# Optimization experiments

Hardware: AMD Instinct MI355X
Metric: run time of the kernel (lower is better)

The kernel has to match this reference:

```python
import jax, jax.numpy as jnp
import numpy as np

# Dims: node hidden = (VO vectors, SO scalars); messages = (VEC_IN vectors, S_M scalars)
VO, SO, VEC_IN, S_M = 16, 100, 17, 132
B, N, K = 4, 2048, 30


def _split(x, nv):
    # flat [..., 3*nv + ns] -> vectors [..., 3, nv], scalars [..., ns]
    v = x[..., :3 * nv].reshape(x.shape[:-1] + (3, nv))
    return v, x[..., 3 * nv:]


def _merge(v, s):
    return jnp.concatenate([v.reshape(v.shape[:-2] + (3 * v.shape[-1],)), s], -1)


def _norm_no_nan(x, axis=-1, keepdims=False, eps=1e-8, sqrt=True):
    out = jnp.maximum(jnp.sum(x * x, axis=axis, keepdims=keepdims), eps)
    return jnp.sqrt(out) if sqrt else out


def _vs_concat(x1, x2, nv1, nv2):
    v1, s1 = _split(x1, nv1)
    v2, s2 = _split(x2, nv2)
    return _merge(jnp.concatenate([v1, v2], -1), jnp.concatenate([s1, s2], -1))


def _gvp(x, nv_in, wh, ws, bs, wv, act=True):
    # Geometric Vector Perceptron: nls=relu on scalars, nlv=sigmoid gate on vector norms.
    v, s = _split(x, nv_in)
    vh = jnp.einsum('...ci,ih->...ch', v, wh)        # c = 3 spatial dims
    vn = _norm_no_nan(vh, axis=-2)                    # [..., h]
    s_out = jnp.concatenate([s, vn], -1) @ ws + bs
    if act:
        s_out = jax.nn.relu(s_out)
    v_out = jnp.einsum('...ch,ho->...co', vh, wv)
    if act:
        v_out = v_out * jax.nn.sigmoid(_norm_no_nan(v_out, axis=-2, keepdims=True))
    return _merge(v_out, s_out)


def _gvp_layernorm(x, nv, gamma, beta, eps=1e-3):
    # scalars: standard LayerNorm (keras default eps=1e-3); vectors: divide by RMS of channel norms
    v, s = _split(x, nv)
    vn2 = _norm_no_nan(v, axis=-2, keepdims=True, sqrt=False)      # [..., 1, nv]
    v = v / jnp.sqrt(jnp.mean(vn2, axis=-1, keepdims=True))
    mu = jnp.mean(s, -1, keepdims=True)
    var = jnp.mean((s - mu) ** 2, -1, keepdims=True)
    s = (s - mu) * jax.lax.rsqrt(var + eps) * gamma + beta
    return _merge(v, s)


def _dense(key, fan_in, fan_out):
    return jax.random.normal(key, (fan_in, fan_out), jnp.float32) / np.sqrt(fan_in)


def setup_inputs() -> dict:
    key = jax.random.key(0)
    ks = jax.random.split(key, 20)
    d = {
        'h_V': jax.random.normal(ks[0], (B, N, 3 * VO + SO), jnp.float32),
        'h_M': jax.random.normal(ks[1], (B, N, K, 3 * VEC_IN + S_M), jnp.float32),
        'mask_V': jnp.ones((B, N), jnp.int32),
        'mask_attend': jnp.ones((B, N, K), jnp.int32),
    }
    # W_EV: GVP(33->16, 232->100), GVP(16->16, 100->100), GVP(16->16, 100->100, no act)
    d['wev1_wh'] = _dense(ks[2], 33, 33)
    d['wev1_ws'] = _dense(ks[3], 232 + 33, 100)
    d['wev1_bs'] = jnp.zeros((100,), jnp.float32)
    d['wev1_wv'] = _dense(ks[4], 33, 16)
    d['wev2_wh'] = _dense(ks[5], 16, 16)
    d['wev2_ws'] = _dense(ks[6], 116, 100)
    d['wev2_bs'] = jnp.zeros((100,), jnp.float32)
    d['wev2_wv'] = _dense(ks[7], 16, 16)
    d['wev3_wh'] = _dense(ks[8], 16, 16)
    d['wev3_ws'] = _dense(ks[9], 116, 100)
    d['wev3_bs'] = jnp.zeros((100,), jnp.float32)
    d['wev3_wv'] = _dense(ks[10], 16, 16)
    # W_dh: GVP(16->32, 100->400), GVP(32->16, 400->100, no act)
    d['wdh1_wh'] = _dense(ks[11], 16, 32)
    d['wdh1_ws'] = _dense(ks[12], 100 + 32, 400)
    d['wdh1_bs'] = jnp.zeros((400,), jnp.float32)
    d['wdh1_wv'] = _dense(ks[13], 32, 32)
    d['wdh2_wh'] = _dense(ks[14], 32, 32)
    d['wdh2_ws'] = _dense(ks[15], 400 + 32, 100)
    d['wdh2_bs'] = jnp.zeros((100,), jnp.float32)
    d['wdh2_wv'] = _dense(ks[16], 32, 16)
    d['ln1_g'] = jnp.ones((100,), jnp.float32)
    d['ln1_b'] = jnp.zeros((100,), jnp.float32)
    d['ln2_g'] = jnp.ones((100,), jnp.float32)
    d['ln2_b'] = jnp.zeros((100,), jnp.float32)
    return d


def reference(h_V, h_M, mask_V, mask_attend,
              wev1_wh, wev1_ws, wev1_bs, wev1_wv,
              wev2_wh, wev2_ws, wev2_bs, wev2_wv,
              wev3_wh, wev3_ws, wev3_bs, wev3_wv,
              wdh1_wh, wdh1_ws, wdh1_bs, wdh1_wv,
              wdh2_wh, wdh2_ws, wdh2_bs, wdh2_wv,
              ln1_g, ln1_b, ln2_g, ln2_b):
    # tile node features along neighbor axis, concat with messages
    h_V_exp = jnp.broadcast_to(h_V[..., None, :], h_M.shape[:-1] + (h_V.shape[-1],))
    h_EV = _vs_concat(h_V_exp, h_M, VO, VEC_IN)                   # [B,N,K, 3*33 + 232]
    m = _gvp(h_EV, VO + VEC_IN, wev1_wh, wev1_ws, wev1_bs, wev1_wv)
    m = _gvp(m, VO, wev2_wh, wev2_ws, wev2_bs, wev2_wv)
    m = _gvp(m, VO, wev3_wh, wev3_ws, wev3_bs, wev3_wv, act=False)
    m = mask_attend[..., None].astype(jnp.float32) * m
    dh = jnp.mean(m, axis=-2)                                     # reduce over neighbors
    hv = _gvp_layernorm(h_V + dh, VO, ln1_g, ln1_b)               # dropout inactive (train=False)
    dh = _gvp(hv, VO, wdh1_wh, wdh1_ws, wdh1_bs, wdh1_wv)
    dh = _gvp(dh, 2 * VO, wdh2_wh, wdh2_ws, wdh2_bs, wdh2_wv, act=False)
    hv = _gvp_layernorm(hv + dh, VO, ln2_g, ln2_b)
    return mask_V[..., None].astype(jnp.float32) * hv
```

## Files before the change

### kernel.cpp

```cpp
#include <hip/hip_runtime.h>
#include <math.h>

#define NT 256

typedef __attribute__((ext_vector_type(8))) short short8;
typedef __attribute__((ext_vector_type(4))) float float4v;

struct P28 {
    const float *h_V, *h_M;
    const int *mask_V, *mask_attend;
    const float *w1h,*w1s,*b1,*w1v;
    const float *w2h,*w2s,*b2,*w2v;
    const float *w3h,*w3s,*b3,*w3v;
    const float *d1h,*d1s,*db1,*d1v;
    const float *d2h,*d2s,*db2,*d2v;
    const float *g1,*be1,*g2,*be2;
    float *out, *dh;
    short *wt1, *wt2, *wt3;
};

__device__ inline short f2bf(float f) {
    union { float f; unsigned u; } v; v.f = f;
    unsigned r = (v.u + 0x7FFFu + ((v.u >> 16) & 1u)) >> 16;
    return (short)r;
}

__device__ void gemm(const float* A0, int split, const float* A1, int KA,
                     const float* uni, int uniK,
                     const float* Bg, int ldB, int N,
                     const float* bias, bool relu,
                     float* outL, int MP, float* Bbuf, int bbf, int tid)
{
    const bool vec = ((N & 3) == 0) && ((ldB & 3) == 0);
    const int Npad = vec ? N : ((N + 3) & ~3);
    const int EQ = MP >> 2;
    const int npairs = EQ * (Npad >> 2);
    const int Ktot = uniK + KA;
    int KC = bbf / Npad;
    if (KC > Ktot) KC = Ktot;

    const bool active = tid < npairs;
    const int e0 = (active ? (tid % EQ) : 0) * 4;
    const int j0 = (active ? (tid / EQ) : 0) * 4;

    float c00=0.f,c01=0.f,c02=0.f,c03=0.f;
    float c10=0.f,c11=0.f,c12=0.f,c13=0.f;
    float c20=0.f,c21=0.f,c22=0.f,c23=0.f;
    float c30=0.f,c31=0.f,c32=0.f,c33=0.f;
    float su0=0.f,su1=0.f,su2=0.f,su3=0.f;

    float4 r0, r1, r2, r3;
    r0.x=r0.y=r0.z=r0.w=0.f; r1=r0; r2=r0; r3=r0;

    if (vec) {
        int kc0 = (KC < Ktot) ? KC : Ktot;
        int nf4 = (kc0 * N) >> 2;
        int f4 = tid;
        if (f4 < nf4) { int f = f4*4; int k = f / N; r0 = *(const float4*)(Bg + (size_t)k*ldB + (f - k*N)); }
        f4 = tid + NT;
        if (f4 < nf4) { int f = f4*4; int k = f / N; r1 = *(const float4*)(Bg + (size_t)k*ldB + (f - k*N)); }
        f4 = tid + 2*NT;
        if (f4 < nf4) { int f = f4*4; int k = f / N; r2 = *(const float4*)(Bg + (size_t)k*ldB + (f - k*N)); }
        f4 = tid + 3*NT;
        if (f4 < nf4) { int f = f4*4; int k = f / N; r3 = *(const float4*)(Bg + (size_t)k*ldB + (f - k*N)); }
    }

    for (int k0 = 0; k0 < Ktot; k0 += KC) {
        int kc = Ktot - k0; if (kc > KC) kc = KC;
        __syncthreads();
        if (vec) {
            int nf4 = (kc * N) >> 2;
            float4* Bb4 = (float4*)Bbuf;
            if (tid        < nf4) Bb4[tid]        = r0;
            if (tid +   NT < nf4) Bb4[tid +   NT] = r1;
            if (tid + 2*NT < nf4) Bb4[tid + 2*NT] = r2;
            if (tid + 3*NT < nf4) Bb4[tid + 3*NT] = r3;
            int k0n = k0 + KC;
            if (k0n < Ktot) {
                int kcn = Ktot - k0n; if (kcn > KC) kcn = KC;
                int nf4n = (kcn * N) >> 2;
                const float* Bn = Bg + (size_t)k0n * ldB;
                int f4 = tid;
                if (f4 < nf4n) { int f = f4*4; int k = f / N; r0 = *(const float4*)(Bn + (size_t)k*ldB + (f - k*N)); }
                f4 = tid + NT;
                if (f4 < nf4n) { int f = f4*4; int k = f / N; r1 = *(const float4*)(Bn + (size_t)k*ldB + (f - k*N)); }
                f4 = tid + 2*NT;
                if (f4 < nf4n) { int f = f4*4; int k = f / N; r2 = *(const float4*)(Bn + (size_t)k*ldB + (f - k*N)); }
                f4 = tid + 3*NT;
                if (f4 < nf4n) { int f = f4*4; int k = f / N; r3 = *(const float4*)(Bn + (size_t)k*ldB + (f - k*N)); }
            }
        } else {
            for (int idx = tid; idx < kc * Npad; idx += NT) {
                int k = idx / Npad, j = idx - k * Npad;
                Bbuf[idx] = (j < N) ? Bg[(size_t)(k0 + k) * ldB + j] : 0.f;
            }
        }
        __syncthreads();
        if (active) {
            for (int k = 0; k < kc; ++k) {
                int kg = k0 + k;
                float4 b4 = *(const float4*)(Bbuf + k * Npad + j0);
                if (kg < uniK) {
                    float u = uni[kg];
                    su0 = fmaf(u, b4.x, su0); su1 = fmaf(u, b4.y, su1);
                    su2 = fmaf(u, b4.z, su2); su3 = fmaf(u, b4.w, su3);
                } else {
                    int ka = kg - uniK;
                    const float* arow = (ka < split) ? (A0 + (size_t)ka * MP + e0)
                                                     : (A1 + (size_t)(ka - split) * MP + e0);
                    float4 a4 = *(const float4*)arow;
                    c00 = fmaf(a4.x, b4.x, c00); c01 = fmaf(a4.y, b4.x, c01);
                    c02 = fmaf(a4.z, b4.x, c02); c03 = fmaf(a4.w, b4.x, c03);
                    c10 = fmaf(a4.x, b4.y, c10); c11 = fmaf(a4.y, b4.y, c11);
                    c12 = fmaf(a4.z, b4.y, c12); c13 = fmaf(a4.w, b4.y, c13);
                    c20 = fmaf(a4.x, b4.z, c20); c21 = fmaf(a4.y, b4.z, c21);
                    c22 = fmaf(a4.z, b4.z, c22); c23 = fmaf(a4.w, b4.z, c23);
                    c30 = fmaf(a4.x, b4.w, c30); c31 = fmaf(a4.y, b4.w, c31);
                    c32 = fmaf(a4.z, b4.w, c32); c33 = fmaf(a4.w, b4.w, c33);
                }
            }
        }
    }
    __syncthreads();
    if (active) {
        float4 o;
        if (j0 + 0 < N) {
            float s = su0 + (bias ? bias[j0 + 0] : 0.f);
            o.x = c00 + s; o.y = c01 + s; o.z = c02 + s; o.w = c03 + s;
            if (relu) { o.x = fmaxf(o.x,0.f); o.y = fmaxf(o.y,0.f); o.z = fmaxf(o.z,0.f); o.w = fmaxf(o.w,0.f); }
            *(float4*)(outL + (size_t)(j0 + 0) * MP + e0) = o;
        }
        if (j0 + 1 < N) {
            float s = su1 + (bias ? bias[j0 + 1] : 0.f);
            o.x = c10 + s; o.y = c11 + s; o.z = c12 + s; o.w = c13 + s;
            if (relu) { o.x = fmaxf(o.x,0.f); o.y = fmaxf(o.y,0.f); o.z = fmaxf(o.z,0.f); o.w = fmaxf(o.w,0.f); }
            *(float4*)(outL + (size_t)(j0 + 1) * MP + e0) = o;
        }
        if (j0 + 2 < N) {
            float s = su2 + (bias ? bias[j0 + 2] : 0.f);
            o.x = c20 + s; o.y = c21 + s; o.z = c22 + s; o.w = c23 + s;
            if (relu) { o.x = fmaxf(o.x,0.f); o.y = fmaxf(o.y,0.f); o.z = fmaxf(o.z,0.f); o.w = fmaxf(o.w,0.f); }
            *(float4*)(outL + (size_t)(j0 + 2) * MP + e0) = o;
        }
        if (j0 + 3 < N) {
            float s = su3 + (bias ? bias[j0 + 3] : 0.f);
            o.x = c30 + s; o.y = c31 + s; o.z = c32 + s; o.w = c33 + s;
            if (relu) { o.x = fmaxf(o.x,0.f); o.y = fmaxf(o.y,0.f); o.z = fmaxf(o.z,0.f); o.w = fmaxf(o.w,0.f); }
            *(float4*)(outL + (size_t)(j0 + 3) * MP + e0) = o;
        }
    }
}

__device__ void vn_dev(const float* vh, int nch, int MP, int cs,
                       float* out, int ostr, int tid)
{
    for (int idx = tid; idx < nch * cs; idx += NT) {
        int h = idx / cs, e = idx - h * cs;
        float a = vh[h * MP + e], b = vh[h * MP + cs + e], c = vh[h * MP + 2 * cs + e];
        out[h * ostr + e] = sqrtf(fmaxf(a * a + b * b + c * c, 1e-8f));
    }
}

__device__ void gate_dev(float* vb, int nch, int MP, int cs, int tid)
{
    for (int idx = tid; idx < nch * cs; idx += NT) {
        int o = idx / cs, e = idx - o * cs;
        float* b = vb + o * MP + e;
        float a = b[0], b1 = b[cs], c = b[2 * cs];
        float n = sqrtf(fmaxf(a * a + b1 * b1 + c * c, 1e-8f));
        float g = 1.f / (1.f + expf(-n));
        b[0] = a * g; b[cs] = b1 * g; b[2 * cs] = c * g;
    }
}

__device__ void mfma_gemm(const short* Alds, int Astr, const short* Bg, int Kpad,
                          int ktiles, const float* bias,
                          short* outA, int outAstr, float* outS, int tid)
{
    const int w = tid >> 6, lane = tid & 63;
    const int q = lane >> 4, l16 = lane & 15;
    for (int t = w; t < 14; t += 4) {
        int mt = t & 1, nt = t >> 1;
        const short* ap = Alds + (mt * 16 + l16) * Astr + q * 8;
        const short* bp = Bg + (size_t)(nt * 16 + l16) * Kpad + q * 8;
        float4v acc = {0.f, 0.f, 0.f, 0.f};
        for (int kt = 0; kt < ktiles; ++kt) {
            short8 a = *(const short8*)(ap + kt * 32);
            short8 b = *(const short8*)(bp + kt * 32);
            acc = __builtin_amdgcn_mfma_f32_16x16x32_bf16(a, b, acc, 0, 0, 0);
        }
        int j = nt * 16 + l16;
        if (j < 100) {
            float bj = bias ? bias[j] : 0.f;
            int ebase = mt * 16 + q * 4;
            for (int r = 0; r < 4; ++r) {
                float v = acc[r] + bj;
                if (outA) { v = fmaxf(v, 0.f); outA[(ebase + r) * outAstr + j] = f2bf(v); }
                else      { outS[j * 33 + (ebase + r)] = v; }
            }
        }
    }
}

__global__ __launch_bounds__(NT) void prep_w(P28 p)
{
    int id = blockIdx.x * NT + threadIdx.x;
    int stride = gridDim.x * NT;
    for (int i = id; i < 112 * 288; i += stride) {
        int n = i / 288, k = i - n * 288;
        float v = 0.f;
        if (n < 100) {
            int row = -1;
            if (k < 132) row = 100 + k;
            else if (k < 165) row = 232 + (k - 132);
            else if (k < 265) row = k - 165;
            if (row >= 0) v = p.w1s[(size_t)row * 100 + n];
        }
        p.wt1[i] = f2bf(v);
    }
    for (int i = id; i < 112 * 128; i += stride) {
        int n = i / 128, k = i - n * 128;
        p.wt2[i] = f2bf((n < 100 && k < 116) ? p.w2s[(size_t)k * 100 + n] : 0.f);
    }
    for (int i = id; i < 112 * 128; i += stride) {
        int n = i / 128, k = i - n * 128;
        p.wt3[i] = f2bf((n < 100 && k < 116) ? p.w3s[(size_t)k * 100 + n] : 0.f);
    }
}

__global__ __launch_bounds__(NT) void edge_kernel(P28 p)
{
    __shared__ __align__(16) float Bbuf[1200];
    __shared__ __align__(16) short A1s[32 * 296];
    __shared__ __align__(16) float bufY[3300];
    __shared__ __align__(16) float vhb[33 * 96];
    __shared__ float maskf[32];

    short* A3s = A1s;
    short* A2s = (short*)bufY;
    float* vbuf = bufY;
    float* S3   = bufY;

    const int node = blockIdx.x, tid = threadIdx.x;
    const float* hV = p.h_V + (size_t)node * 148;

    for (int i = tid; i < 32; i += NT)
        maskf[i] = (i < 30) ? (float)p.mask_attend[(size_t)node * 30 + i] : 0.f;
    for (int idx = tid; idx < 32 * 132; idx += NT) {
        int e = idx / 132, k = idx - e * 132;
        float v = (e < 30) ? p.h_M[((size_t)node * 30 + e) * 183 + 51 + k] : 0.f;
        A1s[e * 296 + k] = f2bf(v);
    }
    for (int idx = tid; idx < 32 * 100; idx += NT) {
        int i = idx >> 5, e = idx & 31;
        A1s[e * 296 + 165 + i] = f2bf(hV[48 + i]);
    }
    for (int idx = tid; idx < 32 * 23; idx += NT) {
        int kk = idx / 32, e = idx - kk * 32;
        A1s[e * 296 + 265 + kk] = 0;
    }
    for (int idx = tid; idx < 33 * 96; idx += NT) {
        int i = idx / 96, r = idx - i * 96, c = r >> 5, e = r & 31;
        float v = 0.f;
        if (i < 16) v = hV[c * 16 + i];
        else if (e < 30) v = p.h_M[((size_t)node * 30 + e) * 183 + c * 17 + (i - 16)];
        vbuf[idx] = v;
    }
    __syncthreads();

    gemm(vbuf, 33, nullptr, 33, nullptr, 0, p.w1h, 33, 33, nullptr, false, vhb, 96, Bbuf, 1200, tid);
    __syncthreads();
    for (int idx = tid; idx < 33 * 32; idx += NT) {
        int h = idx >> 5, e = idx & 31;
        float a = vhb[h * 96 + e], b = vhb[h * 96 + 32 + e], c = vhb[h * 96 + 64 + e];
        A1s[e * 296 + 132 + h] = f2bf(sqrtf(fmaxf(a * a + b * b + c * c, 1e-8f)));
    }
    for (int idx = tid; idx < 32 * 12; idx += NT) {
        int kk = idx >> 5, e = idx & 31;
        A2s[e * 136 + 116 + kk] = 0;
    }
    __syncthreads();
    gemm(vhb, 33, nullptr, 33, nullptr, 0, p.w1v, 16, 16, nullptr, false, vhb, 96, Bbuf, 1200, tid);
    __syncthreads();
    gate_dev(vhb, 16, 96, 32, tid);
    __syncthreads();
    mfma_gemm(A1s, 296, p.wt1, 288, 9, p.b1, A2s, 136, nullptr, tid);
    __syncthreads();

    gemm(vhb, 16, nullptr, 16, nullptr, 0, p.w2h, 16, 16, nullptr, false, vhb + 16 * 96, 96, Bbuf, 1200, tid);
    __syncthreads();
    for (int idx = tid; idx < 16 * 32; idx += NT) {
        int h = idx >> 5, e = idx & 31;
        float a = vhb[(16 + h) * 96 + e], b = vhb[(16 + h) * 96 + 32 + e], c = vhb[(16 + h) * 96 + 64 + e];
        A2s[e * 136 + 100 + h] = f2bf(sqrtf(fmaxf(a * a + b * b + c * c, 1e-8f)));
    }
    for (int idx = tid; idx < 32 * 12; idx += NT) {
        int kk = idx >> 5, e = idx & 31;
        A3s[e * 136 + 116 + kk] = 0;
    }
    __syncthreads();
    gemm(vhb + 16 * 96, 16, nullptr, 16, nullptr, 0, p.w2v, 16, 16, nullptr, false, vhb, 96, Bbuf, 1200, tid);
    __syncthreads();
    gate_dev(vhb, 16, 96, 32, tid);
    __syncthreads();
    mfma_gemm(A2s, 136, p.wt2, 128, 4, p.b2, A3s, 136, nullptr, tid);
    __syncthreads();

    gemm(vhb, 16, nullptr, 16, nullptr, 0, p.w3h, 16, 16, nullptr, false, vhb + 16 * 96, 96, Bbuf, 1200, tid);
    __syncthreads();
    for (int idx = tid; idx < 16 * 32; idx += NT) {
        int h = idx >> 5, e = idx & 31;
        float a = vhb[(16 + h) * 96 + e], b = vhb[(16 + h) * 96 + 32 + e], c = vhb[(16 + h) * 96 + 64 + e];
        A3s[e * 136 + 100 + h] = f2bf(sqrtf(fmaxf(a * a + b * b + c * c, 1e-8f)));
    }
    __syncthreads();
    gemm(vhb + 16 * 96, 16, nullptr, 16, nullptr, 0, p.w3v, 16, 16, nullptr, false, vhb, 96, Bbuf, 1200, tid);
    __syncthreads();
    mfma_gemm(A3s, 136, p.wt3, 128, 4, p.b3, nullptr, 0, S3, tid);
    __syncthreads();

    float* dhn = p.dh + (size_t)node * 148;
    for (int f = tid; f < 148; f += NT) {
        float s = 0.f;
        int e = f % 30;
        if (f < 48) {
            int c = f >> 4, o = f & 15;
            const float* src = vhb + o * 96 + c * 32;
            for (int t = 0; t < 30; ++t) { s += maskf[e] * src[e]; if (++e == 30) e = 0; }
        } else {
            const float* src = S3 + (size_t)(f - 48) * 33;
            for (int t = 0; t < 30; ++t) { s += maskf[e] * src[e]; if (++e == 30) e = 0; }
        }
        dhn[f] = s * (1.f / 30.f);
    }
}

__global__ __launch_bounds__(NT) void node_kernel(P28 p)
{
    __shared__ __align__(16) float Bbuf[3200];
    __shared__ __align__(16) float S1n[132 * 16];
    __shared__ __align__(16) float A2n[400 * 16];
    __shared__ __align__(16) float s2n[100 * 16];
    __shared__ __align__(16) float hvv[16 * 48];
    __shared__ __align__(16) float vhA[32 * 48];
    __shared__ __align__(16) float vhB[32 * 48];
    __shared__ float mu[16], isd[16], vrm[16], mkv[16];

    const int nb = blockIdx.x * 16;
    const int tid = threadIdx.x;

    for (int idx = tid; idx < 1600; idx += NT) {
        int n = idx & 15, j = idx >> 4;
        size_t g = (size_t)(nb + n) * 148 + 48 + j;
        S1n[idx] = p.h_V[g] + p.dh[g];
    }
    for (int idx = tid; idx < 768; idx += NT) {
        int i = idx / 48, r = idx - i * 48, c = r >> 4, n = r & 15;
        size_t g = (size_t)(nb + n) * 148 + c * 16 + i;
        hvv[idx] = p.h_V[g] + p.dh[g];
    }
    for (int i = tid; i < 16; i += NT) mkv[i] = (float)p.mask_V[nb + i];
    __syncthreads();

    if (tid < 16) {
        int n = tid;
        float sm = 0.f;
        for (int j = 0; j < 100; ++j) sm += S1n[j * 16 + n];
        float m = sm * 0.01f, var = 0.f;
        for (int j = 0; j < 100; ++j) { float d = S1n[j * 16 + n] - m; var += d * d; }
        mu[n] = m; isd[n] = rsqrtf(var * 0.01f + 1e-3f);
        float vm = 0.f;
        for (int i = 0; i < 16; ++i) {
            float a = hvv[i * 48 + n], b = hvv[i * 48 + 16 + n], c = hvv[i * 48 + 32 + n];
            vm += fmaxf(a * a + b * b + c * c, 1e-8f);
        }
        vrm[n] = rsqrtf(vm * (1.f / 16.f));
    }
    __syncthreads();
    for (int idx = tid; idx < 1600; idx += NT) {
        int n = idx & 15, j = idx >> 4;
        S1n[idx] = (S1n[idx] - mu[n]) * isd[n] * p.g1[j] + p.be1[j];
    }
    for (int idx = tid; idx < 768; idx += NT) hvv[idx] *= vrm[idx & 15];
    __syncthreads();

    gemm(hvv, 16, nullptr, 16, nullptr, 0, p.d1h, 32, 32, nullptr, false, vhA, 48, Bbuf, 3200, tid);
    __syncthreads();
    vn_dev(vhA, 32, 48, 16, S1n + 100 * 16, 16, tid);
    __syncthreads();
    gemm(S1n, 132, nullptr, 132, nullptr, 0, p.d1s,       400, 200, p.db1,       true, A2n,            16, Bbuf, 3200, tid);
    gemm(S1n, 132, nullptr, 132, nullptr, 0, p.d1s + 200, 400, 200, p.db1 + 200, true, A2n + 200 * 16, 16, Bbuf, 3200, tid);
    gemm(vhA, 32, nullptr, 32, nullptr, 0, p.d1v, 32, 32, nullptr, false, vhB, 48, Bbuf, 3200, tid);
    __syncthreads();
    gate_dev(vhB, 32, 48, 16, tid);
    __syncthreads();

    gemm(vhB, 32, nullptr, 32, nullptr, 0, p.d2h, 32, 32, nullptr, false, vhA, 48, Bbuf, 3200, tid);
    __syncthreads();
    vn_dev(vhA, 32, 48, 16, S1n + 100 * 16, 16, tid);
    __syncthreads();
    gemm(A2n, 400, S1n + 100 * 16, 432, nullptr, 0, p.d2s, 100, 100, p.db2, false, s2n, 16, Bbuf, 3200, tid);
    gemm(vhA, 32, nullptr, 32, nullptr, 0, p.d2v, 16, 16, nullptr, false, vhB, 48, Bbuf, 3200, tid);
    __syncthreads();

    for (int idx = tid; idx < 1600; idx += NT) s2n[idx] += S1n[idx];
    for (int idx = tid; idx < 768; idx += NT) vhB[idx] += hvv[idx];
    __syncthreads();

    if (tid < 16) {
        int n = tid;
        float sm = 0.f;
        for (int j = 0; j < 100; ++j) sm += s2n[j * 16 + n];
        float m = sm * 0.01f, var = 0.f;
        for (int j = 0; j < 100; ++j) { float d = s2n[j * 16 + n] - m; var += d * d; }
        mu[n] = m; isd[n] = rsqrtf(var * 0.01f + 1e-3f);
        float vm = 0.f;
        for (int i = 0; i < 16; ++i) {
            float a = vhB[i * 48 + n], b = vhB[i * 48 + 16 + n], c = vhB[i * 48 + 32 + n];
            vm += fmaxf(a * a + b * b + c * c, 1e-8f);
        }
        vrm[n] = rsqrtf(vm * (1.f / 16.f));
    }
    __syncthreads();
    for (int idx = tid; idx < 1600; idx += NT) {
        int n = idx & 15, j = idx >> 4;
        s2n[idx] = (s2n[idx] - mu[n]) * isd[n] * p.g2[j] + p.be2[j];
    }
    for (int idx = tid; idx < 768; idx += NT) vhB[idx] *= vrm[idx & 15];
    __syncthreads();

    for (int idx = tid; idx < 16 * 148; idx += NT) {
        int n = idx / 148, f = idx - n * 148;
        float v;
        if (f < 48) { int c = f >> 4, o = f & 15; v = vhB[o * 48 + c * 16 + n]; }
        else        { v = s2n[(f - 48) * 16 + n]; }
        p.out[(size_t)(nb + n) * 148 + f] = mkv[n] * v;
    }
}

extern "C" void kernel_launch(void* const* d_in, const int* in_sizes, int n_in,
                              void* d_out, int out_size, void* d_ws, size_t ws_size,
                              hipStream_t stream)
{
    P28 p;
    p.h_V = (const float*)d_in[0];
    p.h_M = (const float*)d_in[1];
    p.mask_V = (const int*)d_in[2];
    p.mask_attend = (const int*)d_in[3];
    const float** w = (const float**)&p.w1h;
    for (int i = 0; i < 24; ++i) w[i] = (const float*)d_in[4 + i];
    p.out = (float*)d_out;
    p.dh  = (float*)d_out;
    p.wt1 = (short*)d_ws;
    p.wt2 = p.wt1 + 112 * 288;
    p.wt3 = p.wt2 + 112 * 128;

    prep_w<<<dim3(64), dim3(NT), 0, stream>>>(p);
    edge_kernel<<<dim3(8192), dim3(NT), 0, stream>>>(p);
    node_kernel<<<dim3(512),  dim3(NT), 0, stream>>>(p);
}
```

Before: 778.2 us.

## Fold per-node scalar term into bias and read small weights directly from global

The node scalar features are identical across all 30 neighbors, so their contribution to the first GVP scalar layer is computed once per node as a bias vector (ubias). This shrinks the MFMA K dimension from 288 to 192. The staged shared-memory GEMM is replaced by gemm_d, which reads weight rows straight from global memory (with w1h padded to 36 columns in prep_w), and two barriers around gate_dev are removed. The cost is a per-node 100x100 fp32 dot-product loop run by only 100 threads, and more scattered global reads of the small weight matrices.

```diff
diff --git a/kernel.cpp b/kernel.cpp
--- a/kernel.cpp
+++ b/kernel.cpp
@@ -17,6 +17,7 @@
     const float *g1,*be1,*g2,*be2;
     float *out, *dh;
     short *wt1, *wt2, *wt3;
+    float *wp1h;
 };
 
 __device__ inline short f2bf(float f) {
@@ -151,6 +152,58 @@
     }
 }
 
+__device__ void gemm_d(const float* A, int Ktot,
+                       const float* Bg, int ldB, int N,
+                       const float* bias, bool relu,
+                       float* outL, int MP, int tid)
+{
+    const int EQ = MP >> 2;
+    const int npairs = EQ * (N >> 2);
+    const bool active = tid < npairs;
+    const int e0 = (active ? (tid % EQ) : 0) * 4;
+    const int j0 = (active ? (tid / EQ) : 0) * 4;
+
+    float c00=0.f,c01=0.f,c02=0.f,c03=0.f;
+    float c10=0.f,c11=0.f,c12=0.f,c13=0.f;
+    float c20=0.f,c21=0.f,c22=0.f,c23=0.f;
+    float c30=0.f,c31=0.f,c32=0.f,c33=0.f;
+
+    if (active) {
+        for (int k = 0; k < Ktot; ++k) {
+            float4 a4 = *(const float4*)(A + (size_t)k * MP + e0);
+            float4 b4 = *(const float4*)(Bg + (size_t)k * ldB + j0);
+            c00 = fmaf(a4.x, b4.x, c00); c01 = fmaf(a4.y, b4.x, c01);
+            c02 = fmaf(a4.z, b4.x, c02); c03 = fmaf(a4.w, b4.x, c03);
+            c10 = fmaf(a4.x, b4.y, c10); c11 = fmaf(a4.y, b4.y, c11);
+            c12 = fmaf(a4.z, b4.y, c12); c13 = fmaf(a4.w, b4.y, c13);
+            c20 = fmaf(a4.x, b4.z, c20); c21 = fmaf(a4.y, b4.z, c21);
+            c22 = fmaf(a4.z, b4.z, c22); c23 = fmaf(a4.w, b4.z, c23);
+            c30 = fmaf(a4.x, b4.w, c30); c31 = fmaf(a4.y, b4.w, c31);
+            c32 = fmaf(a4.z, b4.w, c32); c33 = fmaf(a4.w, b4.w, c33);
+        }
+    }
+    __syncthreads();
+    if (active) {
+        float4 o;
+        float s0 = bias ? bias[j0 + 0] : 0.f;
+        o.x = c00 + s0; o.y = c01 + s0; o.z = c02 + s0; o.w = c03 + s0;
+        if (relu) { o.x = fmaxf(o.x,0.f); o.y = fmaxf(o.y,0.f); o.z = fmaxf(o.z,0.f); o.w = fmaxf(o.w,0.f); }
+        *(float4*)(outL + (size_t)(j0 + 0) * MP + e0) = o;
+        float s1 = bias ? bias[j0 + 1] : 0.f;
+        o.x = c10 + s1; o.y = c11 + s1; o.z = c12 + s1; o.w = c13 + s1;
+        if (relu) { o.x = fmaxf(o.x,0.f); o.y = fmaxf(o.y,0.f); o.z = fmaxf(o.z,0.f); o.w = fmaxf(o.w,0.f); }
+        *(float4*)(outL + (size_t)(j0 + 1) * MP + e0) = o;
+        float s2 = bias ? bias[j0 + 2] : 0.f;
+        o.x = c20 + s2; o.y = c21 + s2; o.z = c22 + s2; o.w = c23 + s2;
+        if (relu) { o.x = fmaxf(o.x,0.f); o.y = fmaxf(o.y,0.f); o.z = fmaxf(o.z,0.f); o.w = fmaxf(o.w,0.f); }
+        *(float4*)(outL + (size_t)(j0 + 2) * MP + e0) = o;
+        float s3 = bias ? bias[j0 + 3] : 0.f;
+        o.x = c30 + s3; o.y = c31 + s3; o.z = c32 + s3; o.w = c33 + s3;
+        if (relu) { o.x = fmaxf(o.x,0.f); o.y = fmaxf(o.y,0.f); o.z = fmaxf(o.z,0.f); o.w = fmaxf(o.w,0.f); }
+        *(float4*)(outL + (size_t)(j0 + 3) * MP + e0) = o;
+    }
+}
+
 __device__ void vn_dev(const float* vh, int nch, int MP, int cs,
                        float* out, int ostr, int tid)
 {
@@ -206,14 +259,13 @@
 {
     int id = blockIdx.x * NT + threadIdx.x;
     int stride = gridDim.x * NT;
-    for (int i = id; i < 112 * 288; i += stride) {
-        int n = i / 288, k = i - n * 288;
+    for (int i = id; i < 112 * 192; i += stride) {
+        int n = i / 192, k = i - n * 192;
         float v = 0.f;
         if (n < 100) {
             int row = -1;
             if (k < 132) row = 100 + k;
             else if (k < 165) row = 232 + (k - 132);
-            else if (k < 265) row = k - 165;
             if (row >= 0) v = p.w1s[(size_t)row * 100 + n];
         }
         p.wt1[i] = f2bf(v);
@@ -226,14 +278,18 @@
         int n = i / 128, k = i - n * 128;
         p.wt3[i] = f2bf((n < 100 && k < 116) ? p.w3s[(size_t)k * 100 + n] : 0.f);
     }
+    for (int i = id; i < 33 * 36; i += stride) {
+        int k = i / 36, j = i - k * 36;
+        p.wp1h[i] = (j < 33) ? p.w1h[(size_t)k * 33 + j] : 0.f;
+    }
 }
 
 __global__ __launch_bounds__(NT) void edge_kernel(P28 p)
 {
-    __shared__ __align__(16) float Bbuf[1200];
-    __shared__ __align__(16) short A1s[32 * 296];
+    __shared__ __align__(16) short A1s[32 * 192];
     __shared__ __align__(16) float bufY[3300];
-    __shared__ __align__(16) float vhb[33 * 96];
+    __shared__ __align__(16) float vhb[36 * 96];
+    __shared__ __align__(16) float ubias[100];
     __shared__ float maskf[32];
 
     short* A3s = A1s;
@@ -249,15 +305,11 @@
     for (int idx = tid; idx < 32 * 132; idx += NT) {
         int e = idx / 132, k = idx - e * 132;
         float v = (e < 30) ? p.h_M[((size_t)node * 30 + e) * 183 + 51 + k] : 0.f;
-        A1s[e * 296 + k] = f2bf(v);
-    }
-    for (int idx = tid; idx < 32 * 100; idx += NT) {
-        int i = idx >> 5, e = idx & 31;
-        A1s[e * 296 + 165 + i] = f2bf(hV[48 + i]);
-    }
-    for (int idx = tid; idx < 32 * 23; idx += NT) {
-        int kk = idx / 32, e = idx - kk * 32;
-        A1s[e * 296 + 265 + kk] = 0;
+        A1s[e * 192 + k] = f2bf(v);
+    }
+    for (int idx = tid; idx < 32 * 27; idx += NT) {
+        int kk = idx >> 5, e = idx & 31;
+        A1s[e * 192 + 165 + kk] = 0;
     }
     for (int idx = tid; idx < 33 * 96; idx += NT) {
         int i = idx / 96, r = idx - i * 96, c = r >> 5, e = r & 31;
@@ -266,28 +318,33 @@
         else if (e < 30) v = p.h_M[((size_t)node * 30 + e) * 183 + c * 17 + (i - 16)];
         vbuf[idx] = v;
     }
-    __syncthreads();
-
-    gemm(vbuf, 33, nullptr, 33, nullptr, 0, p.w1h, 33, 33, nullptr, false, vhb, 96, Bbuf, 1200, tid);
+    for (int j = tid; j < 100; j += NT) {
+        float s = p.b1[j];
+        for (int i = 0; i < 100; ++i)
+            s = fmaf(hV[48 + i], p.w1s[(size_t)i * 100 + j], s);
+        ubias[j] = s;
+    }
+    __syncthreads();
+
+    gemm_d(vbuf, 33, p.wp1h, 36, 36, nullptr, false, vhb, 96, tid);
     __syncthreads();
     for (int idx = tid; idx < 33 * 32; idx += NT) {
         int h = idx >> 5, e = idx & 31;
         float a = vhb[h * 96 + e], b = vhb[h * 96 + 32 + e], c = vhb[h * 96 + 64 + e];
-        A1s[e * 296 + 132 + h] = f2bf(sqrtf(fmaxf(a * a + b * b + c * c, 1e-8f)));
+        A1s[e * 192 + 132 + h] = f2bf(sqrtf(fmaxf(a * a + b * b + c * c, 1e-8f)));
     }
     for (int idx = tid; idx < 32 * 12; idx += NT) {
         int kk = idx >> 5, e = idx & 31;
         A2s[e * 136 + 116 + kk] = 0;
     }
     __syncthreads();
-    gemm(vhb, 33, nullptr, 33, nullptr, 0, p.w1v, 16, 16, nullptr, false, vhb, 96, Bbuf, 1200, tid);
+    gemm_d(vhb, 33, p.w1v, 16, 16, nullptr, false, vhb, 96, tid);
     __syncthreads();
     gate_dev(vhb, 16, 96, 32, tid);
-    __syncthreads();
-    mfma_gemm(A1s, 296, p.wt1, 288, 9, p.b1, A2s, 136, nullptr, tid);
-    __syncthreads();
-
-    gemm(vhb, 16, nullptr, 16, nullptr, 0, p.w2h, 16, 16, nullptr, false, vhb + 16 * 96, 96, Bbuf, 1200, tid);
+    mfma_gemm(A1s, 192, p.wt1, 192, 6, ubias, A2s, 136, nullptr, tid);
+    __syncthreads();
+
+    gemm_d(vhb, 16, p.w2h, 16, 16, nullptr, false, vhb + 16 * 96, 96, tid);
     __syncthreads();
     for (int idx = tid; idx < 16 * 32; idx += NT) {
         int h = idx >> 5, e = idx & 31;
@@ -299,14 +356,13 @@
         A3s[e * 136 + 116 + kk] = 0;
     }
     __syncthreads();
-    gemm(vhb + 16 * 96, 16, nullptr, 16, nullptr, 0, p.w2v, 16, 16, nullptr, false, vhb, 96, Bbuf, 1200, tid);
+    gemm_d(vhb + 16 * 96, 16, p.w2v, 16, 16, nullptr, false, vhb, 96, tid);
     __syncthreads();
     gate_dev(vhb, 16, 96, 32, tid);
-    __syncthreads();
     mfma_gemm(A2s, 136, p.wt2, 128, 4, p.b2, A3s, 136, nullptr, tid);
     __syncthreads();
 
-    gemm(vhb, 16, nullptr, 16, nullptr, 0, p.w3h, 16, 16, nullptr, false, vhb + 16 * 96, 96, Bbuf, 1200, tid);
+    gemm_d(vhb, 16, p.w3h, 16, 16, nullptr, false, vhb + 16 * 96, 96, tid);
     __syncthreads();
     for (int idx = tid; idx < 16 * 32; idx += NT) {
         int h = idx >> 5, e = idx & 31;
@@ -314,7 +370,7 @@
         A3s[e * 136 + 100 + h] = f2bf(sqrtf(fmaxf(a * a + b * b + c * c, 1e-8f)));
     }
     __syncthreads();
-    gemm(vhb + 16 * 96, 16, nullptr, 16, nullptr, 0, p.w3v, 16, 16, nullptr, false, vhb, 96, Bbuf, 1200, tid);
+    gemm_d(vhb + 16 * 96, 16, p.w3v, 16, 16, nullptr, false, vhb, 96, tid);
     __syncthreads();
     mfma_gemm(A3s, 136, p.wt3, 128, 4, p.b3, nullptr, 0, S3, tid);
     __syncthreads();
@@ -452,8 +508,9 @@
     p.out = (float*)d_out;
     p.dh  = (float*)d_out;
     p.wt1 = (short*)d_ws;
-    p.wt2 = p.wt1 + 112 * 288;
+    p.wt2 = p.wt1 + 112 * 192;
     p.wt3 = p.wt2 + 112 * 128;
+    p.wp1h = (float*)(p.wt3 + 112 * 128);
 
     prep_w<<<dim3(64), dim3(NT), 0, stream>>>(p);
     edge_kernel<<<dim3(8192), dim3(NT), 0, stream>>>(p);
```

Result: slower. 823.2 us (+5.8%).

## Fold node-scalar term into per-node bias and fuse masked neighbor reduction into MFMA epilogue

Applied to the files above, without the earlier changes.

The node scalar features are identical for all 30 neighbors, so their product with the first-layer scalar weights is computed once per node as an fp32 bias instead of being tiled into the bf16 A matrix. This shrinks the first MFMA GEMM's K dimension from 288 to 192. The last MFMA GEMM now reduces its masked outputs straight into a shared 100-entry accumulator with LDS atomics, so it no longer writes a full 100x33 tile and reruns the mean. Two barriers are dropped and LDS use is smaller, at the cost of a serial 100-term dot per thread, shared atomics, and a small change in rounding because the node term stays fp32.

```diff
diff --git a/kernel.cpp b/kernel.cpp
--- a/kernel.cpp
+++ b/kernel.cpp
@@ -175,7 +175,8 @@
 
 __device__ void mfma_gemm(const short* Alds, int Astr, const short* Bg, int Kpad,
                           int ktiles, const float* bias,
-                          short* outA, int outAstr, float* outS, int tid)
+                          short* outA, int outAstr,
+                          float* Sred, const float* maskf, int tid)
 {
     const int w = tid >> 6, lane = tid & 63;
     const int q = lane >> 4, l16 = lane & 15;
@@ -193,10 +194,15 @@
         if (j < 100) {
             float bj = bias ? bias[j] : 0.f;
             int ebase = mt * 16 + q * 4;
-            for (int r = 0; r < 4; ++r) {
-                float v = acc[r] + bj;
-                if (outA) { v = fmaxf(v, 0.f); outA[(ebase + r) * outAstr + j] = f2bf(v); }
-                else      { outS[j * 33 + (ebase + r)] = v; }
+            if (outA) {
+                for (int r = 0; r < 4; ++r) {
+                    float v = fmaxf(acc[r] + bj, 0.f);
+                    outA[(ebase + r) * outAstr + j] = f2bf(v);
+                }
+            } else {
+                float part = 0.f;
+                for (int r = 0; r < 4; ++r) part += maskf[ebase + r] * (acc[r] + bj);
+                atomicAdd(&Sred[j], part);
             }
         }
     }
@@ -206,14 +212,13 @@
 {
     int id = blockIdx.x * NT + threadIdx.x;
     int stride = gridDim.x * NT;
-    for (int i = id; i < 112 * 288; i += stride) {
-        int n = i / 288, k = i - n * 288;
+    for (int i = id; i < 112 * 192; i += stride) {
+        int n = i / 192, k = i - n * 192;
         float v = 0.f;
         if (n < 100) {
             int row = -1;
             if (k < 132) row = 100 + k;
             else if (k < 165) row = 232 + (k - 132);
-            else if (k < 265) row = k - 165;
             if (row >= 0) v = p.w1s[(size_t)row * 100 + n];
         }
         p.wt1[i] = f2bf(v);
@@ -230,61 +235,62 @@
 
 __global__ __launch_bounds__(NT) void edge_kernel(P28 p)
 {
+    __shared__ __align__(16) short A1s[32 * 200];
+    __shared__ __align__(16) float vhb[33 * 96];
+    __shared__ __align__(16) short A2s[32 * 136];
     __shared__ __align__(16) float Bbuf[1200];
-    __shared__ __align__(16) short A1s[32 * 296];
-    __shared__ __align__(16) float bufY[3300];
-    __shared__ __align__(16) float vhb[33 * 96];
+    __shared__ float Sred[100];
+    __shared__ float ubias[100];
     __shared__ float maskf[32];
 
     short* A3s = A1s;
-    short* A2s = (short*)bufY;
-    float* vbuf = bufY;
-    float* S3   = bufY;
 
     const int node = blockIdx.x, tid = threadIdx.x;
     const float* hV = p.h_V + (size_t)node * 148;
 
     for (int i = tid; i < 32; i += NT)
         maskf[i] = (i < 30) ? (float)p.mask_attend[(size_t)node * 30 + i] : 0.f;
+    for (int i = tid; i < 100; i += NT) Sred[i] = 0.f;
     for (int idx = tid; idx < 32 * 132; idx += NT) {
         int e = idx / 132, k = idx - e * 132;
         float v = (e < 30) ? p.h_M[((size_t)node * 30 + e) * 183 + 51 + k] : 0.f;
-        A1s[e * 296 + k] = f2bf(v);
-    }
-    for (int idx = tid; idx < 32 * 100; idx += NT) {
-        int i = idx >> 5, e = idx & 31;
-        A1s[e * 296 + 165 + i] = f2bf(hV[48 + i]);
-    }
-    for (int idx = tid; idx < 32 * 23; idx += NT) {
-        int kk = idx / 32, e = idx - kk * 32;
-        A1s[e * 296 + 265 + kk] = 0;
+        A1s[e * 200 + k] = f2bf(v);
+    }
+    for (int idx = tid; idx < 32 * 27; idx += NT) {
+        int kk = idx >> 5, e = idx & 31;
+        A1s[e * 200 + 165 + kk] = 0;
+    }
+    for (int idx = tid; idx < 32 * 12; idx += NT) {
+        int kk = idx >> 5, e = idx & 31;
+        A2s[e * 136 + 116 + kk] = 0;
     }
     for (int idx = tid; idx < 33 * 96; idx += NT) {
         int i = idx / 96, r = idx - i * 96, c = r >> 5, e = r & 31;
         float v = 0.f;
         if (i < 16) v = hV[c * 16 + i];
         else if (e < 30) v = p.h_M[((size_t)node * 30 + e) * 183 + c * 17 + (i - 16)];
-        vbuf[idx] = v;
-    }
-    __syncthreads();
-
-    gemm(vbuf, 33, nullptr, 33, nullptr, 0, p.w1h, 33, 33, nullptr, false, vhb, 96, Bbuf, 1200, tid);
+        vhb[idx] = v;
+    }
+    for (int j = tid; j < 100; j += NT) {
+        float s = p.b1[j];
+        for (int i = 0; i < 100; ++i)
+            s = fmaf(hV[48 + i], p.w1s[(size_t)i * 100 + j], s);
+        ubias[j] = s;
+    }
+    __syncthreads();
+
+    gemm(vhb, 33, nullptr, 33, nullptr, 0, p.w1h, 33, 33, nullptr, false, vhb, 96, Bbuf, 1200, tid);
     __syncthreads();
     for (int idx = tid; idx < 33 * 32; idx += NT) {
         int h = idx >> 5, e = idx & 31;
         float a = vhb[h * 96 + e], b = vhb[h * 96 + 32 + e], c = vhb[h * 96 + 64 + e];
-        A1s[e * 296 + 132 + h] = f2bf(sqrtf(fmaxf(a * a + b * b + c * c, 1e-8f)));
-    }
-    for (int idx = tid; idx < 32 * 12; idx += NT) {
-        int kk = idx >> 5, e = idx & 31;
-        A2s[e * 136 + 116 + kk] = 0;
+        A1s[e * 200 + 132 + h] = f2bf(sqrtf(fmaxf(a * a + b * b + c * c, 1e-8f)));
     }
     __syncthreads();
     gemm(vhb, 33, nullptr, 33, nullptr, 0, p.w1v, 16, 16, nullptr, false, vhb, 96, Bbuf, 1200, tid);
     __syncthreads();
     gate_dev(vhb, 16, 96, 32, tid);
-    __syncthreads();
-    mfma_gemm(A1s, 296, p.wt1, 288, 9, p.b1, A2s, 136, nullptr, tid);
+    mfma_gemm(A1s, 200, p.wt1, 192, 6, ubias, A2s, 136, nullptr, nullptr, tid);
     __syncthreads();
 
     gemm(vhb, 16, nullptr, 16, nullptr, 0, p.w2h, 16, 16, nullptr, false, vhb + 16 * 96, 96, Bbuf, 1200, tid);
@@ -302,8 +308,7 @@
     gemm(vhb + 16 * 96, 16, nullptr, 16, nullptr, 0, p.w2v, 16, 16, nullptr, false, vhb, 96, Bbuf, 1200, tid);
     __syncthreads();
     gate_dev(vhb, 16, 96, 32, tid);
-    __syncthreads();
-    mfma_gemm(A2s, 136, p.wt2, 128, 4, p.b2, A3s, 136, nullptr, tid);
+    mfma_gemm(A2s, 136, p.wt2, 128, 4, p.b2, A3s, 136, nullptr, nullptr, tid);
     __syncthreads();
 
     gemm(vhb, 16, nullptr, 16, nullptr, 0, p.w3h, 16, 16, nullptr, false, vhb + 16 * 96, 96, Bbuf, 1200, tid);
@@ -316,20 +321,21 @@
     __syncthreads();
     gemm(vhb + 16 * 96, 16, nullptr, 16, nullptr, 0, p.w3v, 16, 16, nullptr, false, vhb, 96, Bbuf, 1200, tid);
     __syncthreads();
-    mfma_gemm(A3s, 136, p.wt3, 128, 4, p.b3, nullptr, 0, S3, tid);
+    mfma_gemm(A3s, 136, p.wt3, 128, 4, p.b3, nullptr, 0, Sred, maskf, tid);
     __syncthreads();
 
     float* dhn = p.dh + (size_t)node * 148;
     for (int f = tid; f < 148; f += NT) {
-        float s = 0.f;
-        int e = f % 30;
+        float s;
         if (f < 48) {
             int c = f >> 4, o = f & 15;
             const float* src = vhb + o * 96 + c * 32;
-            for (int t = 0; t < 30; ++t) { s += maskf[e] * src[e]; if (++e == 30) e = 0; }
+            float acc = 0.f;
+            int e = f % 30;
+            for (int t = 0; t < 30; ++t) { acc += maskf[e] * src[e]; if (++e == 30) e = 0; }
+            s = acc;
         } else {
-            const float* src = S3 + (size_t)(f - 48) * 33;
-            for (int t = 0; t < 30; ++t) { s += maskf[e] * src[e]; if (++e == 30) e = 0; }
+            s = Sred[f - 48];
         }
         dhn[f] = s * (1.f / 30.f);
     }
@@ -452,7 +458,7 @@
     p.out = (float*)d_out;
     p.dh  = (float*)d_out;
     p.wt1 = (short*)d_ws;
-    p.wt2 = p.wt1 + 112 * 288;
+    p.wt2 = p.wt1 + 112 * 192;
     p.wt3 = p.wt2 + 112 * 128;
 
     prep_w<<<dim3(64), dim3(NT), 0, stream>>>(p);
```

Result: no change. 782.0 us (+0.5%).
